# Kernel tuning notes

Hardware: AMD Instinct MI355X
Metric: run time of the kernel (lower is better)

## Reference

```python
import jax, jax.numpy as jnp
import numpy as np

D_MODEL = 768
N_HEADS = 12


def setup_inputs() -> dict:
    key = jax.random.key(0)
    ks = jax.random.split(key, 9)
    s = 1.0 / np.sqrt(D_MODEL)
    return {
        "x": jax.random.normal(ks[0], (1, 4096, D_MODEL), dtype=jnp.float32),
        "w_q": jax.random.normal(ks[1], (D_MODEL, D_MODEL), dtype=jnp.float32) * s,
        "b_q": jnp.zeros((D_MODEL,), dtype=jnp.float32),
        "w_k": jax.random.normal(ks[2], (D_MODEL, D_MODEL), dtype=jnp.float32) * s,
        "b_k": jnp.zeros((D_MODEL,), dtype=jnp.float32),
        "w_v": jax.random.normal(ks[3], (D_MODEL, D_MODEL), dtype=jnp.float32) * s,
        "b_v": jnp.zeros((D_MODEL,), dtype=jnp.float32),
        "w_o": jax.random.normal(ks[4], (D_MODEL, D_MODEL), dtype=jnp.float32) * s,
        "b_o": jnp.zeros((D_MODEL,), dtype=jnp.float32),
    }


def reference(x, w_q, b_q, w_k, b_k, w_v, b_v, w_o, b_o):
    b, l, dm = x.shape
    h = N_HEADS
    dk = dm // h
    # projections ([b,l,dm] @ [dm,dm]) then split heads -> [b,h,l,dk]
    def proj(w, bias):
        y = x @ w + bias
        return y.reshape(b, l, h, dk).transpose(0, 2, 1, 3)
    q = proj(w_q, b_q)
    k = proj(w_k, b_k)
    v = proj(w_v, b_v)
    scale = jnp.asarray(dk, x.dtype) ** 0.5
    scores = jnp.einsum("bhqd,bhkd->bhqk", q, k)  # [b,h,l,l]
    causal = jnp.triu(jnp.ones((l, l), dtype=bool), k=1)
    scores = jnp.where(causal, -jnp.inf, scores)
    weights = jax.nn.softmax(scores / scale, axis=-1)
    heads = jnp.einsum("bhqk,bhkd->bhqd", weights, v)  # [b,h,l,dk]
    heads = heads.transpose(0, 2, 1, 3).reshape(b, l, dm)
    return heads @ w_o + b_o
```

## Files before the change

kernel.cpp:

```cpp
#include <hip/hip_runtime.h>

#define L_SEQ 4096
#define DMODEL 768
#define NH 12
#define DK 64

typedef __bf16 bf16;
typedef __bf16 bf16x8 __attribute__((ext_vector_type(8)));
typedef __bf16 bf16x4 __attribute__((ext_vector_type(4)));
typedef float f32x4 __attribute__((ext_vector_type(4)));

#define QSCALE 0.1803368801111204f

__global__ __launch_bounds__(256) void prep_kernel(
    const float* __restrict__ x,
    const float* __restrict__ w_q, const float* __restrict__ w_k,
    const float* __restrict__ w_v, const float* __restrict__ w_o,
    bf16* __restrict__ xb, bf16* __restrict__ wqt, bf16* __restrict__ wkt,
    bf16* __restrict__ wvt, bf16* __restrict__ wot)
{
    const int bid = blockIdx.x;
    const int t = threadIdx.x;
    if (bid < 576) {
        __shared__ bf16 Ls[64][72];
        const int mat = bid / 144;
        const int tile = bid % 144;
        const int k0 = (tile / 12) * 64;
        const int c0 = (tile % 12) * 64;
        const float* W = mat == 0 ? w_q : mat == 1 ? w_k : mat == 2 ? w_v : w_o;
        bf16* WT = mat == 0 ? wqt : mat == 1 ? wkt : mat == 2 ? wvt : wot;
        #pragma unroll
        for (int p = 0; p < 4; ++p) {
            int id = t + p * 256;
            int r = id >> 4, c4 = id & 15;
            float4 v = *(const float4*)(W + (size_t)(k0 + r) * DMODEL + c0 + c4 * 4);
            bf16x4 b; b[0] = (bf16)v.x; b[1] = (bf16)v.y; b[2] = (bf16)v.z; b[3] = (bf16)v.w;
            *(bf16x4*)&Ls[r][c4 * 4] = b;
        }
        __syncthreads();
        #pragma unroll
        for (int p = 0; p < 2; ++p) {
            int id = t + p * 256;
            int crow = id >> 3, kc = id & 7;
            bf16x8 o;
            #pragma unroll
            for (int e = 0; e < 8; ++e) o[e] = Ls[kc * 8 + e][crow];
            *(bf16x8*)(WT + (size_t)(c0 + crow) * DMODEL + k0 + kc * 8) = o;
        }
    } else {
        const size_t base = (size_t)(bid - 576) * 4096;
        #pragma unroll
        for (int p = 0; p < 4; ++p) {
            size_t idx = base + (size_t)(t + p * 256) * 4;
            float4 v = *(const float4*)(x + idx);
            bf16x4 b; b[0] = (bf16)v.x; b[1] = (bf16)v.y; b[2] = (bf16)v.z; b[3] = (bf16)v.w;
            *(bf16x4*)(xb + idx) = b;
        }
    }
}

__global__ __launch_bounds__(256) void proj_kernel(
    const bf16* __restrict__ xb,
    const bf16* __restrict__ wqt, const bf16* __restrict__ wkt, const bf16* __restrict__ wvt,
    const float* __restrict__ b_q, const float* __restrict__ b_k, const float* __restrict__ b_v,
    bf16* __restrict__ qbuf, bf16* __restrict__ kbuf, bf16* __restrict__ vt)
{
    __shared__ bf16 As[128][72];
    __shared__ bf16 Bs[64][72];
    const int t = threadIdx.x;
    const int w = t >> 6, l = t & 63;
    const int lg = l >> 4, lr = l & 15;

    if (blockIdx.x < 768) {
        const int bn = blockIdx.x % 24;
        const int bm = blockIdx.x / 24;
        const int m0 = bm * 128;
        const int gn0 = bn * 64;
        const int sel = gn0 / DMODEL;
        const int c0 = gn0 % DMODEL;
        const bf16* WT = sel ? wkt : wqt;
        const float* bias = sel ? b_k : b_q;
        bf16* dst = sel ? kbuf : qbuf;
        const float scale = sel ? 1.0f : QSCALE;

        f32x4 acc[2][4];
        #pragma unroll
        for (int i = 0; i < 2; i++)
            #pragma unroll
            for (int j = 0; j < 4; j++) acc[i][j] = (f32x4){0.f, 0.f, 0.f, 0.f};

        for (int kk = 0; kk < DMODEL; kk += 64) {
            #pragma unroll
            for (int p = 0; p < 4; ++p) {
                int id = t + p * 256;
                int row = id >> 3, ch = id & 7;
                *(bf16x8*)&As[row][ch * 8] =
                    *(const bf16x8*)(xb + (size_t)(m0 + row) * DMODEL + kk + ch * 8);
            }
            #pragma unroll
            for (int p = 0; p < 2; ++p) {
                int id = t + p * 256;
                int n = id >> 3, ch = id & 7;
                *(bf16x8*)&Bs[n][ch * 8] =
                    *(const bf16x8*)(WT + (size_t)(c0 + n) * DMODEL + kk + ch * 8);
            }
            __syncthreads();
            #pragma unroll
            for (int ks = 0; ks < 2; ++ks) {
                bf16x8 a[2], bfr[4];
                #pragma unroll
                for (int i = 0; i < 2; i++) a[i] = *(const bf16x8*)&As[w * 32 + i * 16 + lr][ks * 32 + lg * 8];
                #pragma unroll
                for (int j = 0; j < 4; j++) bfr[j] = *(const bf16x8*)&Bs[j * 16 + lr][ks * 32 + lg * 8];
                #pragma unroll
                for (int i = 0; i < 2; i++)
                    #pragma unroll
                    for (int j = 0; j < 4; j++)
                        acc[i][j] = __builtin_amdgcn_mfma_f32_16x16x32_bf16(a[i], bfr[j], acc[i][j], 0, 0, 0);
            }
            __syncthreads();
        }
        #pragma unroll
        for (int i = 0; i < 2; i++) {
            #pragma unroll
            for (int j = 0; j < 4; j++) {
                int c = c0 + j * 16 + lr;
                int h = c >> 6, d = c & 63;
                float bb = bias[c];
                #pragma unroll
                for (int r = 0; r < 4; r++) {
                    int m = m0 + w * 32 + i * 16 + lg * 4 + r;
                    float v = (acc[i][j][r] + bb) * scale;
                    dst[((size_t)h * L_SEQ + m) * DK + d] = (bf16)v;
                }
            }
        }
    } else {
        const int bid = blockIdx.x - 768;
        const int bc = bid % 12;
        const int bmm = bid / 12;
        const int c0 = bc * 64;
        const int mm0 = bmm * 128;

        f32x4 acc[8];
        #pragma unroll
        for (int j = 0; j < 8; j++) acc[j] = (f32x4){0.f, 0.f, 0.f, 0.f};

        for (int kk = 0; kk < DMODEL; kk += 64) {
            #pragma unroll
            for (int p = 0; p < 4; ++p) {
                int id = t + p * 256;
                int row = id >> 3, ch = id & 7;
                *(bf16x8*)&As[row][ch * 8] =
                    *(const bf16x8*)(xb + (size_t)(mm0 + row) * DMODEL + kk + ch * 8);
            }
            #pragma unroll
            for (int p = 0; p < 2; ++p) {
                int id = t + p * 256;
                int n = id >> 3, ch = id & 7;
                *(bf16x8*)&Bs[n][ch * 8] =
                    *(const bf16x8*)(wvt + (size_t)(c0 + n) * DMODEL + kk + ch * 8);
            }
            __syncthreads();
            #pragma unroll
            for (int ks = 0; ks < 2; ++ks) {
                bf16x8 a = *(const bf16x8*)&Bs[w * 16 + lr][ks * 32 + lg * 8];
                #pragma unroll
                for (int j = 0; j < 8; j++) {
                    bf16x8 b = *(const bf16x8*)&As[j * 16 + lr][ks * 32 + lg * 8];
                    acc[j] = __builtin_amdgcn_mfma_f32_16x16x32_bf16(a, b, acc[j], 0, 0, 0);
                }
            }
            __syncthreads();
        }
        #pragma unroll
        for (int j = 0; j < 8; j++) {
            int m = mm0 + j * 16 + lr;
            #pragma unroll
            for (int r = 0; r < 4; r++) {
                int c = c0 + w * 16 + lg * 4 + r;
                float v = acc[j][r] + b_v[c];
                vt[(size_t)c * L_SEQ + m] = (bf16)v;
            }
        }
    }
}

__global__ __launch_bounds__(512) void attn_kernel(
    const bf16* __restrict__ qbuf, const bf16* __restrict__ kbuf,
    const bf16* __restrict__ vt, bf16* __restrict__ obuf)
{
    __shared__ __align__(16) char lds[49152];

    const int bid = blockIdx.x;
    const int h  = bid % NH;
    const int qt = 63 - (bid / NH);
    const int q0 = qt * 64;
    const int nt = qt + 1;
    const int nit = (nt + 1) >> 1;

    const int t = threadIdx.x;
    const int w = t >> 6;
    const int g = w >> 2;
    const int wg = w & 3;
    const int l = t & 63;
    const int lg = l >> 4, lr = l & 15;
    const int tg = t & 255;
    const int sw = (lr & 7) << 4;

    char* Kbase = lds + (size_t)g * 8192;
    char* Vbase = lds + 16384 + (size_t)g * 8192;
    char* Pbase = lds + 32768 + (size_t)w * 2048;
    float* mergeAcc = (float*)lds;
    float* mergeMS  = (float*)(lds + 17408);

    const size_t qrow = (size_t)h * L_SEQ + q0 + wg * 16 + lr;
    const bf16x8 qa0 = *(const bf16x8*)(qbuf + qrow * DK + 0  + lg * 8);
    const bf16x8 qa1 = *(const bf16x8*)(qbuf + qrow * DK + 32 + lg * 8);

    f32x4 acc[4];
    #pragma unroll
    for (int j = 0; j < 4; j++) acc[j] = (f32x4){0.f, 0.f, 0.f, 0.f};
    float run_m = -1e30f, run_s = 0.0f;

    const bf16* kb_base = kbuf + (size_t)h * L_SEQ * DK;
    const bf16* vt_base = vt + (size_t)h * DK * L_SEQ;

    bf16x8 k8[2], v8[2];
    if (g < nt) {
        #pragma unroll
        for (int p = 0; p < 2; ++p) {
            int id = tg + p * 256;
            int row = id >> 3, ch = id & 7;
            k8[p] = *(const bf16x8*)(kb_base + (size_t)(g * 64 + row) * DK + ch * 8);
            v8[p] = *(const bf16x8*)(vt_base + (size_t)row * L_SEQ + g * 64 + ch * 8);
        }
    }

    for (int it = 0; it < nit; ++it) {
        const int cur = 2 * it + g;
        const bool active = (cur < nt);
        __syncthreads();
        if (active) {
            #pragma unroll
            for (int p = 0; p < 2; ++p) {
                int id = tg + p * 256;
                int row = id >> 3, ch = id & 7;
                int so = (ch * 16) ^ ((row & 7) << 4);
                *(bf16x8*)(Kbase + row * 128 + so) = k8[p];
                *(bf16x8*)(Vbase + row * 128 + so) = v8[p];
            }
        }
        __syncthreads();
        const int nxt = cur + 2;
        if (nxt < nt) {
            #pragma unroll
            for (int p = 0; p < 2; ++p) {
                int id = tg + p * 256;
                int row = id >> 3, ch = id & 7;
                k8[p] = *(const bf16x8*)(kb_base + (size_t)(nxt * 64 + row) * DK + ch * 8);
                v8[p] = *(const bf16x8*)(vt_base + (size_t)row * L_SEQ + nxt * 64 + ch * 8);
            }
        }
        if (active) {
            f32x4 s[4];
            #pragma unroll
            for (int j = 0; j < 4; j++) s[j] = (f32x4){0.f, 0.f, 0.f, 0.f};
            #pragma unroll
            for (int dh = 0; dh < 2; ++dh) {
                const bf16x8 qa = dh ? qa1 : qa0;
                #pragma unroll
                for (int j = 0; j < 4; j++) {
                    bf16x8 kb = *(const bf16x8*)(Kbase + (j * 16 + lr) * 128 + ((dh * 64 + lg * 16) ^ sw));
                    s[j] = __builtin_amdgcn_mfma_f32_16x16x32_bf16(kb, qa, s[j], 0, 0, 0);
                }
            }
            if (cur == qt) {
                const int qoff = wg * 16 + lr;
                #pragma unroll
                for (int j = 0; j < 4; j++)
                    #pragma unroll
                    for (int r = 0; r < 4; r++)
                        if (j * 16 + lg * 4 + r > qoff) s[j][r] = -3e30f;
            }
            float mx0 = fmaxf(fmaxf(s[0][0], s[0][1]), fmaxf(s[0][2], s[0][3]));
            float mx1 = fmaxf(fmaxf(s[1][0], s[1][1]), fmaxf(s[1][2], s[1][3]));
            float mx2 = fmaxf(fmaxf(s[2][0], s[2][1]), fmaxf(s[2][2], s[2][3]));
            float mx3 = fmaxf(fmaxf(s[3][0], s[3][1]), fmaxf(s[3][2], s[3][3]));
            float mx = fmaxf(fmaxf(mx0, mx1), fmaxf(mx2, mx3));
            mx = fmaxf(mx, __shfl_xor(mx, 16));
            mx = fmaxf(mx, __shfl_xor(mx, 32));
            const float nm = fmaxf(run_m, mx);
            const float scq = exp2f(run_m - nm);
            run_m = nm;
            #pragma unroll
            for (int j = 0; j < 4; j++)
                #pragma unroll
                for (int r = 0; r < 4; r++) s[j][r] = exp2f(s[j][r] - nm);
            float ps0 = (s[0][0] + s[0][1]) + (s[0][2] + s[0][3]);
            float ps1 = (s[1][0] + s[1][1]) + (s[1][2] + s[1][3]);
            float ps2 = (s[2][0] + s[2][1]) + (s[2][2] + s[2][3]);
            float ps3 = (s[3][0] + s[3][1]) + (s[3][2] + s[3][3]);
            float ps = (ps0 + ps1) + (ps2 + ps3);
            ps += __shfl_xor(ps, 16);
            ps += __shfl_xor(ps, 32);
            run_s = run_s * scq + ps;
            #pragma unroll
            for (int j = 0; j < 4; j++) {
                bf16x4 pk;
                pk[0] = (bf16)s[j][0]; pk[1] = (bf16)s[j][1];
                pk[2] = (bf16)s[j][2]; pk[3] = (bf16)s[j][3];
                *(bf16x4*)(Pbase + lr * 128 + ((j * 32 + lg * 8) ^ sw)) = pk;
            }
            if (!__all(scq == 1.0f)) {
                float sc0 = __shfl(scq, lg * 4 + 0);
                float sc1 = __shfl(scq, lg * 4 + 1);
                float sc2 = __shfl(scq, lg * 4 + 2);
                float sc3 = __shfl(scq, lg * 4 + 3);
                #pragma unroll
                for (int jd = 0; jd < 4; jd++) {
                    acc[jd][0] *= sc0; acc[jd][1] *= sc1;
                    acc[jd][2] *= sc2; acc[jd][3] *= sc3;
                }
            }
            #pragma unroll
            for (int dh = 0; dh < 2; ++dh) {
                bf16x8 pa = *(const bf16x8*)(Pbase + lr * 128 + ((dh * 64 + lg * 16) ^ sw));
                #pragma unroll
                for (int jd = 0; jd < 4; jd++) {
                    bf16x8 vb = *(const bf16x8*)(Vbase + (jd * 16 + lr) * 128 + ((dh * 64 + lg * 16) ^ sw));
                    acc[jd] = __builtin_amdgcn_mfma_f32_16x16x32_bf16(pa, vb, acc[jd], 0, 0, 0);
                }
            }
        }
    }

    __syncthreads();
    if (g == 1) {
        float* base = mergeAcc + (size_t)(wg * 64 + l) * 17;
        #pragma unroll
        for (int jd = 0; jd < 4; jd++)
            #pragma unroll
            for (int r = 0; r < 4; r++) base[jd * 4 + r] = acc[jd][r];
        mergeMS[(wg * 64 + l) * 2 + 0] = run_m;
        mergeMS[(wg * 64 + l) * 2 + 1] = run_s;
    }
    __syncthreads();
    if (g == 0) {
        const float* base = mergeAcc + (size_t)(wg * 64 + l) * 17;
        const float mB = mergeMS[(wg * 64 + l) * 2 + 0];
        const float sB = mergeMS[(wg * 64 + l) * 2 + 1];
        const float mF = fmaxf(run_m, mB);
        const float sa = exp2f(run_m - mF);
        const float sb = exp2f(mB - mF);
        const float sT = run_s * sa + sB * sb;
        float a4[4], b4[4], rs[4];
        #pragma unroll
        for (int r = 0; r < 4; r++) {
            a4[r] = __shfl(sa, lg * 4 + r);
            b4[r] = __shfl(sb, lg * 4 + r);
            rs[r] = __shfl(sT, lg * 4 + r);
        }
        #pragma unroll
        for (int jd = 0; jd < 4; jd++) {
            #pragma unroll
            for (int r = 0; r < 4; r++) {
                float v = acc[jd][r] * a4[r] + base[jd * 4 + r] * b4[r];
                int m = q0 + wg * 16 + lg * 4 + r;
                obuf[(size_t)m * DMODEL + h * DK + jd * 16 + lr] = (bf16)(v / rs[r]);
            }
        }
    }
}

__global__ __launch_bounds__(256) void out_proj_kernel(
    const bf16* __restrict__ obuf, const bf16* __restrict__ wot,
    const float* __restrict__ b_o, float* __restrict__ out)
{
    __shared__ bf16 As[128][72];
    __shared__ bf16 Bts[64][72];
    const int bn = blockIdx.x % 12;
    const int bm = blockIdx.x / 12;
    const int m0 = bm * 128, c0 = bn * 64;
    const int t = threadIdx.x;
    const int w = t >> 6, l = t & 63, lg = l >> 4, lr = l & 15;

    f32x4 acc[2][4];
    #pragma unroll
    for (int i = 0; i < 2; i++)
        #pragma unroll
        for (int j = 0; j < 4; j++) acc[i][j] = (f32x4){0.f, 0.f, 0.f, 0.f};

    for (int kk = 0; kk < DMODEL; kk += 64) {
        #pragma unroll
        for (int p = 0; p < 4; ++p) {
            int id = t + p * 256;
            int row = id >> 3, ch = id & 7;
            *(bf16x8*)&As[row][ch * 8] =
                *(const bf16x8*)(obuf + (size_t)(m0 + row) * DMODEL + kk + ch * 8);
        }
        #pragma unroll
        for (int p = 0; p < 2; ++p) {
            int id = t + p * 256;
            int n = id >> 3, ch = id & 7;
            *(bf16x8*)&Bts[n][ch * 8] =
                *(const bf16x8*)(wot + (size_t)(c0 + n) * DMODEL + kk + ch * 8);
        }
        __syncthreads();
        #pragma unroll
        for (int ks = 0; ks < 2; ++ks) {
            bf16x8 a[2], bfr[4];
            #pragma unroll
            for (int i = 0; i < 2; i++) a[i] = *(const bf16x8*)&As[w * 32 + i * 16 + lr][ks * 32 + lg * 8];
            #pragma unroll
            for (int j = 0; j < 4; j++) bfr[j] = *(const bf16x8*)&Bts[j * 16 + lr][ks * 32 + lg * 8];
            #pragma unroll
            for (int i = 0; i < 2; i++)
                #pragma unroll
                for (int j = 0; j < 4; j++)
                    acc[i][j] = __builtin_amdgcn_mfma_f32_16x16x32_bf16(a[i], bfr[j], acc[i][j], 0, 0, 0);
        }
        __syncthreads();
    }
    #pragma unroll
    for (int i = 0; i < 2; i++) {
        #pragma unroll
        for (int j = 0; j < 4; j++) {
            int c = c0 + j * 16 + lr;
            float bb = b_o[c];
            #pragma unroll
            for (int r = 0; r < 4; r++) {
                int m = m0 + w * 32 + i * 16 + lg * 4 + r;
                out[(size_t)m * DMODEL + c] = acc[i][j][r] + bb;
            }
        }
    }
}

extern "C" void kernel_launch(void* const* d_in, const int* in_sizes, int n_in,
                              void* d_out, int out_size, void* d_ws, size_t ws_size,
                              hipStream_t stream) {
    const float* x   = (const float*)d_in[0];
    const float* w_q = (const float*)d_in[1];
    const float* b_q = (const float*)d_in[2];
    const float* w_k = (const float*)d_in[3];
    const float* b_k = (const float*)d_in[4];
    const float* w_v = (const float*)d_in[5];
    const float* b_v = (const float*)d_in[6];
    const float* w_o = (const float*)d_in[7];
    const float* b_o = (const float*)d_in[8];
    float* out = (float*)d_out;

    char* ws = (char*)d_ws;
    const size_t SZ = (size_t)NH * L_SEQ * DK * sizeof(bf16);
    const size_t WTSZ = (size_t)DMODEL * DMODEL * sizeof(bf16);
    bf16* qbuf = (bf16*)(ws);
    bf16* kbuf = (bf16*)(ws + SZ);
    bf16* vt   = (bf16*)(ws + 2 * SZ);
    bf16* obuf = (bf16*)(ws + 3 * SZ);
    bf16* xb   = (bf16*)(ws + 4 * SZ);
    bf16* wqt  = (bf16*)(ws + 5 * SZ);
    bf16* wkt  = (bf16*)(ws + 5 * SZ + WTSZ);
    bf16* wvt  = (bf16*)(ws + 5 * SZ + 2 * WTSZ);
    bf16* wot  = (bf16*)(ws + 5 * SZ + 3 * WTSZ);

    prep_kernel<<<dim3(1344), dim3(256), 0, stream>>>(x, w_q, w_k, w_v, w_o, xb, wqt, wkt, wvt, wot);
    proj_kernel<<<dim3(1152), dim3(256), 0, stream>>>(xb, wqt, wkt, wvt, b_q, b_k, b_v, qbuf, kbuf, vt);
    attn_kernel<<<dim3(768), dim3(512), 0, stream>>>(qbuf, kbuf, vt, obuf);
    out_proj_kernel<<<dim3(384), dim3(256), 0, stream>>>(obuf, wot, b_o, out);
}
```

Before: 123.6 us.

## Defer softmax rescaling, compute row sums via MFMA, add MFMA priority hints

```diff
diff --git a/kernel.cpp b/kernel.cpp
--- a/kernel.cpp
+++ b/kernel.cpp
@@ -11,6 +11,7 @@
 typedef float f32x4 __attribute__((ext_vector_type(4)));
 
 #define QSCALE 0.1803368801111204f
+#define DEFER_THR 8.0f
 
 __global__ __launch_bounds__(256) void prep_kernel(
     const float* __restrict__ x,
@@ -212,16 +213,21 @@
     char* Vbase = lds + 16384 + (size_t)g * 8192;
     char* Pbase = lds + 32768 + (size_t)w * 2048;
     float* mergeAcc = (float*)lds;
-    float* mergeMS  = (float*)(lds + 17408);
+    float* mergeM   = (float*)(lds + 22528);
 
     const size_t qrow = (size_t)h * L_SEQ + q0 + wg * 16 + lr;
     const bf16x8 qa0 = *(const bf16x8*)(qbuf + qrow * DK + 0  + lg * 8);
     const bf16x8 qa1 = *(const bf16x8*)(qbuf + qrow * DK + 32 + lg * 8);
 
+    bf16x8 ones;
+    #pragma unroll
+    for (int e = 0; e < 8; ++e) ones[e] = (bf16)1.0f;
+
     f32x4 acc[4];
     #pragma unroll
     for (int j = 0; j < 4; j++) acc[j] = (f32x4){0.f, 0.f, 0.f, 0.f};
-    float run_m = -1e30f, run_s = 0.0f;
+    f32x4 acc_sum = (f32x4){0.f, 0.f, 0.f, 0.f};
+    float run_m = -1e30f;
 
     const bf16* kb_base = kbuf + (size_t)h * L_SEQ * DK;
     const bf16* vt_base = vt + (size_t)h * DK * L_SEQ;
@@ -266,6 +272,7 @@
             f32x4 s[4];
             #pragma unroll
             for (int j = 0; j < 4; j++) s[j] = (f32x4){0.f, 0.f, 0.f, 0.f};
+            __builtin_amdgcn_s_setprio(1);
             #pragma unroll
             for (int dh = 0; dh < 2; ++dh) {
                 const bf16x8 qa = dh ? qa1 : qa0;
@@ -275,6 +282,7 @@
                     s[j] = __builtin_amdgcn_mfma_f32_16x16x32_bf16(kb, qa, s[j], 0, 0, 0);
                 }
             }
+            __builtin_amdgcn_s_setprio(0);
             if (cur == qt) {
                 const int qoff = wg * 16 + lr;
                 #pragma unroll
@@ -283,28 +291,36 @@
                     for (int r = 0; r < 4; r++)
                         if (j * 16 + lg * 4 + r > qoff) s[j][r] = -3e30f;
             }
-            float mx0 = fmaxf(fmaxf(s[0][0], s[0][1]), fmaxf(s[0][2], s[0][3]));
-            float mx1 = fmaxf(fmaxf(s[1][0], s[1][1]), fmaxf(s[1][2], s[1][3]));
-            float mx2 = fmaxf(fmaxf(s[2][0], s[2][1]), fmaxf(s[2][2], s[2][3]));
-            float mx3 = fmaxf(fmaxf(s[3][0], s[3][1]), fmaxf(s[3][2], s[3][3]));
-            float mx = fmaxf(fmaxf(mx0, mx1), fmaxf(mx2, mx3));
+            float m0 = fmaxf(fmaxf(s[0][0], s[0][1]), s[0][2]);
+            float m1 = fmaxf(fmaxf(s[0][3], s[1][0]), s[1][1]);
+            float m2 = fmaxf(fmaxf(s[1][2], s[1][3]), s[2][0]);
+            float m3 = fmaxf(fmaxf(s[2][1], s[2][2]), s[2][3]);
+            float m4 = fmaxf(fmaxf(s[3][0], s[3][1]), s[3][2]);
+            float t1 = fmaxf(fmaxf(m0, m1), m2);
+            float t2 = fmaxf(fmaxf(m3, m4), s[3][3]);
+            float mx = fmaxf(t1, t2);
             mx = fmaxf(mx, __shfl_xor(mx, 16));
             mx = fmaxf(mx, __shfl_xor(mx, 32));
-            const float nm = fmaxf(run_m, mx);
-            const float scq = exp2f(run_m - nm);
-            run_m = nm;
+            if (!__all(mx <= run_m + DEFER_THR)) {
+                const float nm = fmaxf(run_m, mx);
+                const float scq = exp2f(run_m - nm);
+                run_m = nm;
+                float sc0 = __shfl(scq, lg * 4 + 0);
+                float sc1 = __shfl(scq, lg * 4 + 1);
+                float sc2 = __shfl(scq, lg * 4 + 2);
+                float sc3 = __shfl(scq, lg * 4 + 3);
+                #pragma unroll
+                for (int jd = 0; jd < 4; jd++) {
+                    acc[jd][0] *= sc0; acc[jd][1] *= sc1;
+                    acc[jd][2] *= sc2; acc[jd][3] *= sc3;
+                }
+                acc_sum[0] *= sc0; acc_sum[1] *= sc1;
+                acc_sum[2] *= sc2; acc_sum[3] *= sc3;
+            }
             #pragma unroll
             for (int j = 0; j < 4; j++)
                 #pragma unroll
-                for (int r = 0; r < 4; r++) s[j][r] = exp2f(s[j][r] - nm);
-            float ps0 = (s[0][0] + s[0][1]) + (s[0][2] + s[0][3]);
-            float ps1 = (s[1][0] + s[1][1]) + (s[1][2] + s[1][3]);
-            float ps2 = (s[2][0] + s[2][1]) + (s[2][2] + s[2][3]);
-            float ps3 = (s[3][0] + s[3][1]) + (s[3][2] + s[3][3]);
-            float ps = (ps0 + ps1) + (ps2 + ps3);
-            ps += __shfl_xor(ps, 16);
-            ps += __shfl_xor(ps, 32);
-            run_s = run_s * scq + ps;
+                for (int r = 0; r < 4; r++) s[j][r] = exp2f(s[j][r] - run_m);
             #pragma unroll
             for (int j = 0; j < 4; j++) {
                 bf16x4 pk;
@@ -312,62 +328,53 @@
                 pk[2] = (bf16)s[j][2]; pk[3] = (bf16)s[j][3];
                 *(bf16x4*)(Pbase + lr * 128 + ((j * 32 + lg * 8) ^ sw)) = pk;
             }
-            if (!__all(scq == 1.0f)) {
-                float sc0 = __shfl(scq, lg * 4 + 0);
-                float sc1 = __shfl(scq, lg * 4 + 1);
-                float sc2 = __shfl(scq, lg * 4 + 2);
-                float sc3 = __shfl(scq, lg * 4 + 3);
-                #pragma unroll
-                for (int jd = 0; jd < 4; jd++) {
-                    acc[jd][0] *= sc0; acc[jd][1] *= sc1;
-                    acc[jd][2] *= sc2; acc[jd][3] *= sc3;
-                }
-            }
+            __builtin_amdgcn_s_setprio(1);
             #pragma unroll
             for (int dh = 0; dh < 2; ++dh) {
                 bf16x8 pa = *(const bf16x8*)(Pbase + lr * 128 + ((dh * 64 + lg * 16) ^ sw));
+                acc_sum = __builtin_amdgcn_mfma_f32_16x16x32_bf16(pa, ones, acc_sum, 0, 0, 0);
                 #pragma unroll
                 for (int jd = 0; jd < 4; jd++) {
                     bf16x8 vb = *(const bf16x8*)(Vbase + (jd * 16 + lr) * 128 + ((dh * 64 + lg * 16) ^ sw));
                     acc[jd] = __builtin_amdgcn_mfma_f32_16x16x32_bf16(pa, vb, acc[jd], 0, 0, 0);
                 }
             }
+            __builtin_amdgcn_s_setprio(0);
         }
     }
 
     __syncthreads();
     if (g == 1) {
-        float* base = mergeAcc + (size_t)(wg * 64 + l) * 17;
+        float* base = mergeAcc + (size_t)(wg * 64 + l) * 21;
         #pragma unroll
         for (int jd = 0; jd < 4; jd++)
             #pragma unroll
             for (int r = 0; r < 4; r++) base[jd * 4 + r] = acc[jd][r];
-        mergeMS[(wg * 64 + l) * 2 + 0] = run_m;
-        mergeMS[(wg * 64 + l) * 2 + 1] = run_s;
+        #pragma unroll
+        for (int r = 0; r < 4; r++) base[16 + r] = acc_sum[r];
+        mergeM[wg * 64 + l] = run_m;
     }
     __syncthreads();
     if (g == 0) {
-        const float* base = mergeAcc + (size_t)(wg * 64 + l) * 17;
-        const float mB = mergeMS[(wg * 64 + l) * 2 + 0];
-        const float sB = mergeMS[(wg * 64 + l) * 2 + 1];
+        const float* base = mergeAcc + (size_t)(wg * 64 + l) * 21;
+        const float mB = mergeM[wg * 64 + l];
         const float mF = fmaxf(run_m, mB);
         const float sa = exp2f(run_m - mF);
         const float sb = exp2f(mB - mF);
-        const float sT = run_s * sa + sB * sb;
-        float a4[4], b4[4], rs[4];
+        float a4[4], b4[4];
         #pragma unroll
         for (int r = 0; r < 4; r++) {
             a4[r] = __shfl(sa, lg * 4 + r);
             b4[r] = __shfl(sb, lg * 4 + r);
-            rs[r] = __shfl(sT, lg * 4 + r);
         }
         #pragma unroll
         for (int jd = 0; jd < 4; jd++) {
             #pragma unroll
             for (int r = 0; r < 4; r++) {
+                float denom = acc_sum[r] * a4[r] + base[16 + r] * b4[r];
                 float v = acc[jd][r] * a4[r] + base[jd * 4 + r] * b4[r];
                 int m = q0 + wg * 16 + lg * 4 + r;
-                obuf[(size_t)m * DMODEL + h * DK + jd * 16 + lr] = (bf16)(v / rs[r]);
+                obuf[(size_t)m * DMODEL + h * DK + jd * 16 + lr] = (bf16)(v / denom);
             }
         }
     }
```

Result: faster. 115.3 us (-6.7%).
